# Optimization experiments

Hardware: AMD Instinct MI355X
Metric: run time of the kernel (lower is better)

## Reference

```python
import jax, jax.numpy as jnp
import numpy as np
import math

B, T, D = 4, 2048, 1024
NHEAD = 16
HEAD_DIM = D // NHEAD
MAX_REL = 16  # max_relative_position default


def setup_inputs() -> dict:
    key = jax.random.key(0)
    ks = jax.random.split(key, 10)
    s = 1.0 / math.sqrt(D)
    inp = {
        "x": jax.random.normal(ks[0], (B, T, D), dtype=jnp.float32),
        "Wq": jax.random.normal(ks[1], (D, D), dtype=jnp.float32) * s,
        "bq": jnp.zeros((D,), dtype=jnp.float32),
        "Wk": jax.random.normal(ks[2], (D, D), dtype=jnp.float32) * s,
        "bk": jnp.zeros((D,), dtype=jnp.float32),
        "Wv": jax.random.normal(ks[3], (D, D), dtype=jnp.float32) * s,
        "bv": jnp.zeros((D,), dtype=jnp.float32),
        "rel_bias": jax.random.normal(ks[4], (2 * MAX_REL - 1, NHEAD), dtype=jnp.float32) * 0.02,
        "Wo": jax.random.normal(ks[5], (D, D), dtype=jnp.float32) * s,
        "bo": jnp.zeros((D,), dtype=jnp.float32),
    }
    return inp


def _relative_bias(rel_bias, seq_len):
    # distance matrix clamped to [-(MAX_REL-1), MAX_REL-1], shifted to index table
    r = jnp.arange(seq_len)
    dist = jnp.clip(r[None, :] - r[:, None], -MAX_REL + 1, MAX_REL - 1) + MAX_REL - 1
    # gather: [T, T, H] -> [H, T, T]
    return jnp.transpose(rel_bias[dist], (2, 0, 1))


def reference(x, Wq, bq, Wk, bk, Wv, bv, rel_bias, Wo, bo):
    Bdim, Tdim, Ddim = x.shape
    # torch Linear: x @ W.T + b
    Q = x @ Wq.T + bq
    K = x @ Wk.T + bk
    V = x @ Wv.T + bv
    # [B, H, T, hd]
    Q = Q.reshape(Bdim, Tdim, NHEAD, HEAD_DIM).transpose(0, 2, 1, 3)
    K = K.reshape(Bdim, Tdim, NHEAD, HEAD_DIM).transpose(0, 2, 1, 3)
    V = V.reshape(Bdim, Tdim, NHEAD, HEAD_DIM).transpose(0, 2, 1, 3)
    scores = jnp.einsum("bhqd,bhkd->bhqk", Q, K) / math.sqrt(HEAD_DIM)
    scores = scores + _relative_bias(rel_bias, Tdim)[None]  # [1,H,T,T]
    attn = jax.nn.softmax(scores, axis=-1)
    out = jnp.einsum("bhqk,bhkd->bhqd", attn, V)
    out = out.transpose(0, 2, 1, 3).reshape(Bdim, Tdim, Ddim)
    return out @ Wo.T + bo
```

## Files before the change

kernel.cpp:

```cpp
#include <hip/hip_runtime.h>
#include <stdint.h>
#include <math.h>

typedef unsigned short u16;
typedef __bf16 bf16x8 __attribute__((ext_vector_type(8)));
typedef float f32x4 __attribute__((ext_vector_type(4)));
typedef float f32x2 __attribute__((ext_vector_type(2)));
typedef unsigned short u16x8 __attribute__((ext_vector_type(8)));
typedef unsigned short u16x4 __attribute__((ext_vector_type(4)));

#define BATCH 4
#define SEQT 2048
#define DMODEL 1024
#define NHEAD 16
#define HDIM 64
#define LOG2E 1.44269504f

#define LDS_GLD16(gp, lp)                                                     \
  __builtin_amdgcn_global_load_lds(                                           \
      (const __attribute__((address_space(1))) void*)(gp),                    \
      (__attribute__((address_space(3))) void*)(lp), 16, 0, 0)

static __device__ __forceinline__ u16 f2bf(float f) {
  union { float f; uint32_t u; } c; c.f = f;
  uint32_t u = c.u;
  return (u16)((u + 0x7fffu + ((u >> 16) & 1u)) >> 16);
}
static __device__ __forceinline__ u16 f2bf_fast(float f) {
  union { float f; uint32_t u; } c; c.f = f;
  return (u16)((c.u + 0x8000u) >> 16);
}
static __device__ __forceinline__ uint32_t pkbf(float a, float b) {
  union { float f; uint32_t u; } ca, cb; ca.f = a; cb.f = b;
  return __builtin_amdgcn_perm(cb.u + 0x8000u, ca.u + 0x8000u, 0x07060302u);
}

__global__ __launch_bounds__(256) void k_convert(const float* __restrict__ s,
                                                 u16* __restrict__ d, int n4) {
  int i = blockIdx.x * 256 + threadIdx.x;
  if (i >= n4) return;
  float4 v = ((const float4*)s)[i];
  u16x4 o = {f2bf(v.x), f2bf(v.y), f2bf(v.z), f2bf(v.w)};
  ((u16x4*)d)[i] = o;
}

__global__ __launch_bounds__(256) void k_gemm_qkv(
    const u16* __restrict__ A, const u16* __restrict__ W0,
    const u16* __restrict__ W1, const u16* __restrict__ W2,
    const float* __restrict__ b0, const float* __restrict__ b1,
    const float* __restrict__ b2, u16* __restrict__ dq, u16* __restrict__ dk,
    u16* __restrict__ dv) {
  __shared__ u16 As[128 * 64];
  __shared__ u16 Bs[128 * 64];

  const int z = blockIdx.z;
  const u16* Bm = z == 0 ? W0 : (z == 1 ? W1 : W2);
  const float* bias = z == 0 ? b0 : (z == 1 ? b1 : b2);
  u16* dst = z == 0 ? dq : (z == 1 ? dk : dv);

  const int tid = threadIdx.x;
  const int wave = tid >> 6, lane = tid & 63;
  const int quad = lane >> 4, l16 = lane & 15;
  const int wm = wave & 1, wn = wave >> 1;
  const int m0 = blockIdx.x * 128, n0 = blockIdx.y * 128;
  const int lrow = lane >> 3, lcol = (lane & 7) * 8;

  f32x4 acc[4][4] = {};

  for (int kt = 0; kt < 1024; kt += 64) {
    __syncthreads();
    for (int c = 0; c < 4; ++c) {
      int rr = (wave * 4 + c) * 8 + lrow;
      LDS_GLD16(A + (size_t)(m0 + rr) * 1024 + kt + lcol,
                &As[(wave * 4 + c) * 512]);
      LDS_GLD16(Bm + (size_t)(n0 + rr) * 1024 + kt + lcol,
                &Bs[(wave * 4 + c) * 512]);
    }
    __syncthreads();
    for (int kh = 0; kh < 2; ++kh) {
      bf16x8 af[4], bfr[4];
      for (int mt = 0; mt < 4; ++mt)
        af[mt] = *(const bf16x8*)&As[(wm * 64 + mt * 16 + l16) * 64 + kh * 32 +
                                     quad * 8];
      for (int nt = 0; nt < 4; ++nt)
        bfr[nt] = *(const bf16x8*)&Bs[(wn * 64 + nt * 16 + l16) * 64 + kh * 32 +
                                      quad * 8];
      for (int mt = 0; mt < 4; ++mt)
        for (int nt = 0; nt < 4; ++nt)
          acc[mt][nt] = __builtin_amdgcn_mfma_f32_16x16x32_bf16(
              af[mt], bfr[nt], acc[mt][nt], 0, 0, 0);
    }
  }

  for (int mt = 0; mt < 4; ++mt)
    for (int nt = 0; nt < 4; ++nt) {
      int n = n0 + wn * 64 + nt * 16 + l16;
      float bv = bias[n];
      int h = n >> 6, hd = n & 63;
      for (int r = 0; r < 4; ++r) {
        int m = m0 + wm * 64 + mt * 16 + quad * 4 + r;
        int b = m >> 11, t = m & 2047;
        float v = acc[mt][nt][r] + bv;
        dst[(((size_t)b * NHEAD + h) * SEQT + t) * HDIM + hd] = f2bf_fast(v);
      }
    }
}

__global__ __launch_bounds__(256) void k_gemm_proj(const u16* __restrict__ A,
                                                   const u16* __restrict__ Bm,
                                                   const float* __restrict__ bias,
                                                   float* __restrict__ out) {
  __shared__ u16 As[128 * 64];
  __shared__ u16 Bs[128 * 64];

  const int tid = threadIdx.x;
  const int wave = tid >> 6, lane = tid & 63;
  const int quad = lane >> 4, l16 = lane & 15;
  const int wm = wave & 1, wn = wave >> 1;
  const int m0 = blockIdx.x * 128, n0 = blockIdx.y * 128;
  const int lrow = lane >> 3, lcol = (lane & 7) * 8;

  f32x4 acc[4][4] = {};

  for (int kt = 0; kt < 1024; kt += 64) {
    __syncthreads();
    for (int c = 0; c < 4; ++c) {
      int rr = (wave * 4 + c) * 8 + lrow;
      LDS_GLD16(A + (size_t)(m0 + rr) * 1024 + kt + lcol,
                &As[(wave * 4 + c) * 512]);
      LDS_GLD16(Bm + (size_t)(n0 + rr) * 1024 + kt + lcol,
                &Bs[(wave * 4 + c) * 512]);
    }
    __syncthreads();
    for (int kh = 0; kh < 2; ++kh) {
      bf16x8 af[4], bfr[4];
      for (int mt = 0; mt < 4; ++mt)
        af[mt] = *(const bf16x8*)&As[(wm * 64 + mt * 16 + l16) * 64 + kh * 32 +
                                     quad * 8];
      for (int nt = 0; nt < 4; ++nt)
        bfr[nt] = *(const bf16x8*)&Bs[(wn * 64 + nt * 16 + l16) * 64 + kh * 32 +
                                      quad * 8];
      for (int mt = 0; mt < 4; ++mt)
        for (int nt = 0; nt < 4; ++nt)
          acc[mt][nt] = __builtin_amdgcn_mfma_f32_16x16x32_bf16(
              af[mt], bfr[nt], acc[mt][nt], 0, 0, 0);
    }
  }

  for (int mt = 0; mt < 4; ++mt)
    for (int nt = 0; nt < 4; ++nt) {
      int n = n0 + wn * 64 + nt * 16 + l16;
      float bv = bias[n];
      for (int r = 0; r < 4; ++r) {
        int m = m0 + wm * 64 + mt * 16 + quad * 4 + r;
        out[(size_t)m * 1024 + n] = acc[mt][nt][r] + bv;
      }
    }
}

__global__ __launch_bounds__(256) void k_attn(const u16* __restrict__ Qb,
                                              const u16* __restrict__ Kb,
                                              const u16* __restrict__ Vb,
                                              const float* __restrict__ relb,
                                              u16* __restrict__ Obf) {
  __shared__ u16 Ks[64 * 64];
  __shared__ u16 VTs[64 * 72];
  __shared__ u16 Ps[4][32 * 72];
  __shared__ float biasL[32];

  const int tid = threadIdx.x;
  const int wave = tid >> 6, lane = tid & 63;
  const int quad = lane >> 4, l16 = lane & 15;
  const int qt = blockIdx.x;
  const int bh = blockIdx.y;
  const int h = bh & (NHEAD - 1);
  const size_t base = (size_t)bh * SEQT * HDIM;
  const int q0 = qt * 128;
  const int qbase = q0 + wave * 32;

  if (tid < 31) biasL[tid] = relb[tid * NHEAD + h] * LOG2E;
  const float bLo = relb[0 * NHEAD + h] * LOG2E;
  const float bHi = relb[30 * NHEAD + h] * LOG2E;
  const float CL = 0.125f * LOG2E;

  bf16x8 bq[2][2];
  for (int qg = 0; qg < 2; ++qg) {
    const u16* qp = Qb + base + (size_t)(qbase + qg * 16 + l16) * HDIM;
    bq[qg][0] = *(const bf16x8*)(qp + quad * 8);
    bq[qg][1] = *(const bf16x8*)(qp + 32 + quad * 8);
  }

  f32x4 Oacc[4][2] = {};
  f32x2 ls2[2] = {};

  const int kp = tid >> 3;
  const int dgw = tid & 7;
  uint32_t* VT32 = (uint32_t*)VTs;

  for (int kt2 = 0; kt2 < 32; ++kt2) {
    const int k0 = kt2 * 64;
    __syncthreads();

    for (int c = 0; c < 2; ++c) {
      int rl = lane >> 3;
      int row = (wave * 2 + c) * 8 + rl;
      int gb = (lane & 7) ^ rl;
      LDS_GLD16(Kb + base + (size_t)(k0 + row) * HDIM + gb * 8,
                &Ks[(wave * 2 + c) * 512]);
    }
    {
      const u16* vp = Vb + base + (size_t)(k0 + 2 * kp) * HDIM + dgw * 8;
      u16x8 v0 = *(const u16x8*)vp;
      u16x8 v1 = *(const u16x8*)(vp + HDIM);
      const uint32_t* a32 = (const uint32_t*)&v0;
      const uint32_t* b32 = (const uint32_t*)&v1;
      int col = (((kp >> 2) ^ dgw) << 2) + (kp & 3);
      for (int j2 = 0; j2 < 4; ++j2) {
        uint32_t lo = __builtin_amdgcn_perm(a32[j2], b32[j2], 0x01000504u);
        uint32_t hi = __builtin_amdgcn_perm(a32[j2], b32[j2], 0x03020706u);
        int d0 = dgw * 8 + 2 * j2;
        VT32[d0 * 36 + col] = lo;
        VT32[(d0 + 1) * 36 + col] = hi;
      }
    }
    __syncthreads();

    for (int kg = 0; kg < 4; ++kg) {
      const int krow = kg * 16 + l16;
      const int sl = krow & 7;
      bf16x8 ak0 = *(const bf16x8*)&Ks[krow * 64 + ((quad ^ sl) << 3)];
      bf16x8 ak1 = *(const bf16x8*)&Ks[krow * 64 + (((quad + 4) ^ sl) << 3)];
      const int kb = k0 + kg * 16;
      for (int qg = 0; qg < 2; ++qg) {
        f32x4 s = {};
        s = __builtin_amdgcn_mfma_f32_16x16x32_bf16(ak0, bq[qg][0], s, 0, 0, 0);
        s = __builtin_amdgcn_mfma_f32_16x16x32_bf16(ak1, bq[qg][1], s, 0, 0, 0);
        const int qa = qbase + qg * 16;
        float p0, p1, p2, p3;
        const int dmin = kb - (qa + 15);
        const int dmax = kb + 15 - qa;
        if (dmin >= 15 || dmax <= -15) {
          const float ub = (dmin >= 15) ? bHi : bLo;
          p0 = __builtin_amdgcn_exp2f(fmaf(s[0], CL, ub));
          p1 = __builtin_amdgcn_exp2f(fmaf(s[1], CL, ub));
          p2 = __builtin_amdgcn_exp2f(fmaf(s[2], CL, ub));
          p3 = __builtin_amdgcn_exp2f(fmaf(s[3], CL, ub));
        } else {
          const int db = kb + quad * 4 - (qa + l16);
          float pv[4];
          for (int r = 0; r < 4; ++r) {
            int d = db + r;
            d = d < -15 ? -15 : (d > 15 ? 15 : d);
            pv[r] = __builtin_amdgcn_exp2f(fmaf(s[r], CL, biasL[d + 15]));
          }
          p0 = pv[0]; p1 = pv[1]; p2 = pv[2]; p3 = pv[3];
        }
        f32x2 t01 = {p0, p1}, t23 = {p2, p3};
        ls2[qg] += t01 + t23;
        uint2 w;
        w.x = pkbf(p0, p1);
        w.y = pkbf(p2, p3);
        *(uint2*)&Ps[wave][(qg * 16 + l16) * 72 + kg * 16 + quad * 4] = w;
      }
    }

    bf16x8 bp[2][2];
    for (int qg = 0; qg < 2; ++qg)
      for (int kh = 0; kh < 2; ++kh)
        bp[qg][kh] = *(const bf16x8*)&Ps[wave][(qg * 16 + l16) * 72 + kh * 32 +
                                              quad * 8];
    for (int dg = 0; dg < 4; ++dg) {
      const int d = dg * 16 + l16;
      const int g = d >> 3;
      bf16x8 av0 = *(const bf16x8*)&VTs[d * 72 + ((quad ^ g) << 3)];
      bf16x8 av1 = *(const bf16x8*)&VTs[d * 72 + (((quad + 4) ^ g) << 3)];
      for (int qg = 0; qg < 2; ++qg) {
        Oacc[dg][qg] = __builtin_amdgcn_mfma_f32_16x16x32_bf16(
            av0, bp[qg][0], Oacc[dg][qg], 0, 0, 0);
        Oacc[dg][qg] = __builtin_amdgcn_mfma_f32_16x16x32_bf16(
            av1, bp[qg][1], Oacc[dg][qg], 0, 0, 0);
      }
    }
  }

  float rinv[2];
  for (int qg = 0; qg < 2; ++qg) {
    float v = ls2[qg].x + ls2[qg].y;
    v += __shfl_xor(v, 16, 64);
    v += __shfl_xor(v, 32, 64);
    rinv[qg] = 1.0f / v;
  }

  const int b = bh >> 4;
  for (int dg = 0; dg < 4; ++dg)
    for (int qg = 0; qg < 2; ++qg) {
      int t = qbase + qg * 16 + l16;
      float o0 = Oacc[dg][qg][0] * rinv[qg];
      float o1 = Oacc[dg][qg][1] * rinv[qg];
      float o2 = Oacc[dg][qg][2] * rinv[qg];
      float o3 = Oacc[dg][qg][3] * rinv[qg];
      uint2 w;
      w.x = pkbf(o0, o1);
      w.y = pkbf(o2, o3);
      *(uint2*)(Obf + ((size_t)(b * SEQT + t)) * DMODEL + h * HDIM + dg * 16 +
                quad * 4) = w;
    }
}

extern "C" void kernel_launch(void* const* d_in, const int* in_sizes, int n_in,
                              void* d_out, int out_size, void* d_ws,
                              size_t ws_size, hipStream_t stream) {
  const float* x = (const float*)d_in[0];
  const float* Wq = (const float*)d_in[1];
  const float* bq = (const float*)d_in[2];
  const float* Wk = (const float*)d_in[3];
  const float* bk = (const float*)d_in[4];
  const float* Wv = (const float*)d_in[5];
  const float* bv = (const float*)d_in[6];
  const float* relb = (const float*)d_in[7];
  const float* Wo = (const float*)d_in[8];
  const float* bo = (const float*)d_in[9];
  float* out = (float*)d_out;

  char* ws = (char*)d_ws;
  const size_t SZ_X = (size_t)BATCH * SEQT * DMODEL * 2;
  const size_t SZ_W = (size_t)DMODEL * DMODEL * 2;
  u16* xbf = (u16*)(ws);
  u16* Wqb = (u16*)(ws + SZ_X);
  u16* Wkb = (u16*)(ws + SZ_X + SZ_W);
  u16* Wvb = (u16*)(ws + SZ_X + 2 * SZ_W);
  u16* Wob = (u16*)(ws + SZ_X + 3 * SZ_W);
  u16* Qb = (u16*)(ws + SZ_X + 4 * SZ_W);
  u16* Kb = (u16*)(ws + 2 * SZ_X + 4 * SZ_W);
  u16* Vb = (u16*)(ws + 3 * SZ_X + 4 * SZ_W);
  u16* Obf = (u16*)(ws + 4 * SZ_X + 4 * SZ_W);

  const int NX = BATCH * SEQT * DMODEL;
  const int NW = DMODEL * DMODEL;
  k_convert<<<NX / 4 / 256, 256, 0, stream>>>(x, xbf, NX / 4);
  k_convert<<<NW / 4 / 256, 256, 0, stream>>>(Wq, Wqb, NW / 4);
  k_convert<<<NW / 4 / 256, 256, 0, stream>>>(Wk, Wkb, NW / 4);
  k_convert<<<NW / 4 / 256, 256, 0, stream>>>(Wv, Wvb, NW / 4);
  k_convert<<<NW / 4 / 256, 256, 0, stream>>>(Wo, Wob, NW / 4);

  k_gemm_qkv<<<dim3(64, 8, 3), 256, 0, stream>>>(xbf, Wqb, Wkb, Wvb, bq, bk,
                                                 bv, Qb, Kb, Vb);
  k_attn<<<dim3(16, 64), 256, 0, stream>>>(Qb, Kb, Vb, relb, Obf);
  k_gemm_proj<<<dim3(64, 8), 256, 0, stream>>>(Obf, Wob, bo, out);
}
```

Measured before the change: 343.1 us.

## Produce transposed V from GEMM, widen attention to 512 threads, fuse converts

Merges the five fp32-to-bf16 conversion launches into one kernel. Splits the QKV projection into a Q/K GEMM and a separate V GEMM that writes V already transposed per head (Wv·xᵀ), so attention can load V tiles straight into LDS with async global-to-LDS loads instead of transposing with register permutes each iteration. Attention now runs 8 waves of 16 queries each instead of 4 waves of 32, which gives more waves per block at the cost of each K/V tile being reused across fewer queries per wave. The transposed V store in the GEMM epilogue writes scattered 2-byte values and may cost some write efficiency.

```diff
diff --git a/kernel.cpp b/kernel.cpp
--- a/kernel.cpp
+++ b/kernel.cpp
@@ -35,28 +35,36 @@
   return __builtin_amdgcn_perm(cb.u + 0x8000u, ca.u + 0x8000u, 0x07060302u);
 }
 
-__global__ __launch_bounds__(256) void k_convert(const float* __restrict__ s,
-                                                 u16* __restrict__ d, int n4) {
+__global__ __launch_bounds__(256) void k_convert_all(
+    const float* __restrict__ x, const float* __restrict__ Wq,
+    const float* __restrict__ Wk, const float* __restrict__ Wv,
+    const float* __restrict__ Wo, u16* __restrict__ xbf,
+    u16* __restrict__ Wqkv, u16* __restrict__ Wob) {
+  const int NX4 = 2097152, NW4 = 262144;
   int i = blockIdx.x * 256 + threadIdx.x;
-  if (i >= n4) return;
-  float4 v = ((const float4*)s)[i];
+  const float* s; u16* d; int js, jd;
+  if (i < NX4) {
+    s = x; d = xbf; js = jd = i;
+  } else if (i < NX4 + 3 * NW4) {
+    int j = i - NX4;
+    int w = j >> 18;
+    s = (w == 0) ? Wq : (w == 1) ? Wk : Wv;
+    js = j & (NW4 - 1);
+    d = Wqkv; jd = j;
+  } else {
+    s = Wo; d = Wob; js = jd = i - NX4 - 3 * NW4;
+  }
+  float4 v = ((const float4*)s)[js];
   u16x4 o = {f2bf(v.x), f2bf(v.y), f2bf(v.z), f2bf(v.w)};
-  ((u16x4*)d)[i] = o;
-}
-
-__global__ __launch_bounds__(256) void k_gemm_qkv(
-    const u16* __restrict__ A, const u16* __restrict__ W0,
-    const u16* __restrict__ W1, const u16* __restrict__ W2,
-    const float* __restrict__ b0, const float* __restrict__ b1,
-    const float* __restrict__ b2, u16* __restrict__ dq, u16* __restrict__ dk,
-    u16* __restrict__ dv) {
+  ((u16x4*)d)[jd] = o;
+}
+
+__global__ __launch_bounds__(256) void k_gemm_qk(
+    const u16* __restrict__ A, const u16* __restrict__ Bqk,
+    const float* __restrict__ bq_, const float* __restrict__ bk_,
+    u16* __restrict__ dq, u16* __restrict__ dk) {
   __shared__ u16 As[128 * 64];
   __shared__ u16 Bs[128 * 64];
-
-  const int z = blockIdx.z;
-  const u16* Bm = z == 0 ? W0 : (z == 1 ? W1 : W2);
-  const float* bias = z == 0 ? b0 : (z == 1 ? b1 : b2);
-  u16* dst = z == 0 ? dq : (z == 1 ? dk : dv);
 
   const int tid = threadIdx.x;
   const int wave = tid >> 6, lane = tid & 63;
@@ -73,7 +81,7 @@
       int rr = (wave * 4 + c) * 8 + lrow;
       LDS_GLD16(A + (size_t)(m0 + rr) * 1024 + kt + lcol,
                 &As[(wave * 4 + c) * 512]);
-      LDS_GLD16(Bm + (size_t)(n0 + rr) * 1024 + kt + lcol,
+      LDS_GLD16(Bqk + (size_t)(n0 + rr) * 1024 + kt + lcol,
                 &Bs[(wave * 4 + c) * 512]);
     }
     __syncthreads();
@@ -92,16 +100,75 @@
     }
   }
 
+  u16* dst = (n0 < 1024) ? dq : dk;
+  const float* bias = (n0 < 1024) ? bq_ : bk_;
+  for (int mt = 0; mt < 4; ++mt)
+    for (int nt = 0; nt < 4; ++nt) {
+      int nn = (n0 + wn * 64 + nt * 16 + l16) & 1023;
+      float bv = bias[nn];
+      int h = nn >> 6, hd = nn & 63;
+      for (int r = 0; r < 4; ++r) {
+        int m = m0 + wm * 64 + mt * 16 + quad * 4 + r;
+        int b = m >> 11, t = m & 2047;
+        dst[(((size_t)b * NHEAD + h) * SEQT + t) * HDIM + hd] =
+            f2bf_fast(acc[mt][nt][r] + bv);
+      }
+    }
+}
+
+__global__ __launch_bounds__(256) void k_gemm_vt(const u16* __restrict__ A,
+                                                 const u16* __restrict__ Bx,
+                                                 const float* __restrict__ bv_,
+                                                 u16* __restrict__ Vt) {
+  __shared__ u16 As[128 * 64];
+  __shared__ u16 Bs[128 * 64];
+  __shared__ float biasS[128];
+
+  const int tid = threadIdx.x;
+  const int wave = tid >> 6, lane = tid & 63;
+  const int quad = lane >> 4, l16 = lane & 15;
+  const int wm = wave & 1, wn = wave >> 1;
+  const int m0 = blockIdx.x * 128, n0 = blockIdx.y * 128;
+  const int lrow = lane >> 3, lcol = (lane & 7) * 8;
+
+  if (tid < 128) biasS[tid] = bv_[m0 + tid];
+
+  f32x4 acc[4][4] = {};
+
+  for (int kt = 0; kt < 1024; kt += 64) {
+    __syncthreads();
+    for (int c = 0; c < 4; ++c) {
+      int rr = (wave * 4 + c) * 8 + lrow;
+      LDS_GLD16(A + (size_t)(m0 + rr) * 1024 + kt + lcol,
+                &As[(wave * 4 + c) * 512]);
+      LDS_GLD16(Bx + (size_t)(n0 + rr) * 1024 + kt + lcol,
+                &Bs[(wave * 4 + c) * 512]);
+    }
+    __syncthreads();
+    for (int kh = 0; kh < 2; ++kh) {
+      bf16x8 af[4], bfr[4];
+      for (int mt = 0; mt < 4; ++mt)
+        af[mt] = *(const bf16x8*)&As[(wm * 64 + mt * 16 + l16) * 64 + kh * 32 +
+                                     quad * 8];
+      for (int nt = 0; nt < 4; ++nt)
+        bfr[nt] = *(const bf16x8*)&Bs[(wn * 64 + nt * 16 + l16) * 64 + kh * 32 +
+                                      quad * 8];
+      for (int mt = 0; mt < 4; ++mt)
+        for (int nt = 0; nt < 4; ++nt)
+          acc[mt][nt] = __builtin_amdgcn_mfma_f32_16x16x32_bf16(
+              af[mt], bfr[nt], acc[mt][nt], 0, 0, 0);
+    }
+  }
+
   for (int mt = 0; mt < 4; ++mt)
     for (int nt = 0; nt < 4; ++nt) {
       int n = n0 + wn * 64 + nt * 16 + l16;
-      float bv = bias[n];
-      int h = n >> 6, hd = n & 63;
+      int b = n >> 11, t = n & 2047;
       for (int r = 0; r < 4; ++r) {
         int m = m0 + wm * 64 + mt * 16 + quad * 4 + r;
-        int b = m >> 11, t = m & 2047;
-        float v = acc[mt][nt][r] + bv;
-        dst[(((size_t)b * NHEAD + h) * SEQT + t) * HDIM + hd] = f2bf_fast(v);
+        float v = acc[mt][nt][r] + biasS[m - m0];
+        Vt[((size_t)(b * NHEAD + (m >> 6)) * HDIM + (m & 63)) * SEQT + t] =
+            f2bf_fast(v);
       }
     }
 }
@@ -158,14 +225,14 @@
     }
 }
 
-__global__ __launch_bounds__(256) void k_attn(const u16* __restrict__ Qb,
-                                              const u16* __restrict__ Kb,
-                                              const u16* __restrict__ Vb,
-                                              const float* __restrict__ relb,
-                                              u16* __restrict__ Obf) {
+__global__ __launch_bounds__(512, 8) void k_attn(const u16* __restrict__ Qb,
+                                                 const u16* __restrict__ Kb,
+                                                 const u16* __restrict__ Vt,
+                                                 const float* __restrict__ relb,
+                                                 u16* __restrict__ Obf) {
   __shared__ u16 Ks[64 * 64];
-  __shared__ u16 VTs[64 * 72];
-  __shared__ u16 Ps[4][32 * 72];
+  __shared__ u16 VTs[64 * 64];
+  __shared__ u16 Ps[8][16 * 72];
   __shared__ float biasL[32];
 
   const int tid = threadIdx.x;
@@ -176,135 +243,99 @@
   const int h = bh & (NHEAD - 1);
   const size_t base = (size_t)bh * SEQT * HDIM;
   const int q0 = qt * 128;
-  const int qbase = q0 + wave * 32;
+  const int qa = q0 + wave * 16;
 
   if (tid < 31) biasL[tid] = relb[tid * NHEAD + h] * LOG2E;
   const float bLo = relb[0 * NHEAD + h] * LOG2E;
   const float bHi = relb[30 * NHEAD + h] * LOG2E;
   const float CL = 0.125f * LOG2E;
 
-  bf16x8 bq[2][2];
-  for (int qg = 0; qg < 2; ++qg) {
-    const u16* qp = Qb + base + (size_t)(qbase + qg * 16 + l16) * HDIM;
-    bq[qg][0] = *(const bf16x8*)(qp + quad * 8);
-    bq[qg][1] = *(const bf16x8*)(qp + 32 + quad * 8);
-  }
-
-  f32x4 Oacc[4][2] = {};
-  f32x2 ls2[2] = {};
-
-  const int kp = tid >> 3;
-  const int dgw = tid & 7;
-  uint32_t* VT32 = (uint32_t*)VTs;
+  bf16x8 bq0, bq1;
+  {
+    const u16* qp = Qb + base + (size_t)(qa + l16) * HDIM;
+    bq0 = *(const bf16x8*)(qp + quad * 8);
+    bq1 = *(const bf16x8*)(qp + 32 + quad * 8);
+  }
+
+  f32x4 Oacc[4] = {};
+  f32x2 ls2 = {};
+
+  const int rl = lane >> 3;
+  const int gb = (lane & 7) ^ rl;
+  const int srow = wave * 8 + rl;
+  const u16* kgp = Kb + base + (size_t)srow * HDIM + gb * 8;
+  const u16* vgp = Vt + base + (size_t)srow * SEQT + gb * 8;
+  u16* ksl = &Ks[wave * 512];
+  u16* vsl = &VTs[wave * 512];
+  const int sl = l16 & 7;
 
   for (int kt2 = 0; kt2 < 32; ++kt2) {
     const int k0 = kt2 * 64;
     __syncthreads();
-
-    for (int c = 0; c < 2; ++c) {
-      int rl = lane >> 3;
-      int row = (wave * 2 + c) * 8 + rl;
-      int gb = (lane & 7) ^ rl;
-      LDS_GLD16(Kb + base + (size_t)(k0 + row) * HDIM + gb * 8,
-                &Ks[(wave * 2 + c) * 512]);
-    }
-    {
-      const u16* vp = Vb + base + (size_t)(k0 + 2 * kp) * HDIM + dgw * 8;
-      u16x8 v0 = *(const u16x8*)vp;
-      u16x8 v1 = *(const u16x8*)(vp + HDIM);
-      const uint32_t* a32 = (const uint32_t*)&v0;
-      const uint32_t* b32 = (const uint32_t*)&v1;
-      int col = (((kp >> 2) ^ dgw) << 2) + (kp & 3);
-      for (int j2 = 0; j2 < 4; ++j2) {
-        uint32_t lo = __builtin_amdgcn_perm(a32[j2], b32[j2], 0x01000504u);
-        uint32_t hi = __builtin_amdgcn_perm(a32[j2], b32[j2], 0x03020706u);
-        int d0 = dgw * 8 + 2 * j2;
-        VT32[d0 * 36 + col] = lo;
-        VT32[(d0 + 1) * 36 + col] = hi;
-      }
-    }
+    LDS_GLD16(kgp + (size_t)k0 * HDIM, ksl);
+    LDS_GLD16(vgp + k0, vsl);
     __syncthreads();
 
     for (int kg = 0; kg < 4; ++kg) {
       const int krow = kg * 16 + l16;
-      const int sl = krow & 7;
       bf16x8 ak0 = *(const bf16x8*)&Ks[krow * 64 + ((quad ^ sl) << 3)];
-      bf16x8 ak1 = *(const bf16x8*)&Ks[krow * 64 + (((quad + 4) ^ sl) << 3)];
+      bf16x8 ak1 = *(const bf16x8*)&Ks[krow * 64 + (((4 + quad) ^ sl) << 3)];
+      f32x4 s = {};
+      s = __builtin_amdgcn_mfma_f32_16x16x32_bf16(ak0, bq0, s, 0, 0, 0);
+      s = __builtin_amdgcn_mfma_f32_16x16x32_bf16(ak1, bq1, s, 0, 0, 0);
       const int kb = k0 + kg * 16;
-      for (int qg = 0; qg < 2; ++qg) {
-        f32x4 s = {};
-        s = __builtin_amdgcn_mfma_f32_16x16x32_bf16(ak0, bq[qg][0], s, 0, 0, 0);
-        s = __builtin_amdgcn_mfma_f32_16x16x32_bf16(ak1, bq[qg][1], s, 0, 0, 0);
-        const int qa = qbase + qg * 16;
-        float p0, p1, p2, p3;
-        const int dmin = kb - (qa + 15);
-        const int dmax = kb + 15 - qa;
-        if (dmin >= 15 || dmax <= -15) {
-          const float ub = (dmin >= 15) ? bHi : bLo;
-          p0 = __builtin_amdgcn_exp2f(fmaf(s[0], CL, ub));
-          p1 = __builtin_amdgcn_exp2f(fmaf(s[1], CL, ub));
-          p2 = __builtin_amdgcn_exp2f(fmaf(s[2], CL, ub));
-          p3 = __builtin_amdgcn_exp2f(fmaf(s[3], CL, ub));
-        } else {
-          const int db = kb + quad * 4 - (qa + l16);
-          float pv[4];
-          for (int r = 0; r < 4; ++r) {
-            int d = db + r;
-            d = d < -15 ? -15 : (d > 15 ? 15 : d);
-            pv[r] = __builtin_amdgcn_exp2f(fmaf(s[r], CL, biasL[d + 15]));
-          }
-          p0 = pv[0]; p1 = pv[1]; p2 = pv[2]; p3 = pv[3];
+      float p0, p1, p2, p3;
+      const int dmin = kb - (qa + 15);
+      const int dmax = kb + 15 - qa;
+      if (dmin >= 15 || dmax <= -15) {
+        const float ub = (dmin >= 15) ? bHi : bLo;
+        p0 = __builtin_amdgcn_exp2f(fmaf(s[0], CL, ub));
+        p1 = __builtin_amdgcn_exp2f(fmaf(s[1], CL, ub));
+        p2 = __builtin_amdgcn_exp2f(fmaf(s[2], CL, ub));
+        p3 = __builtin_amdgcn_exp2f(fmaf(s[3], CL, ub));
+      } else {
+        const int db = kb + quad * 4 - (qa + l16);
+        float pv[4];
+        for (int r = 0; r < 4; ++r) {
+          int d = db + r;
+          d = d < -15 ? -15 : (d > 15 ? 15 : d);
+          pv[r] = __builtin_amdgcn_exp2f(fmaf(s[r], CL, biasL[d + 15]));
         }
-        f32x2 t01 = {p0, p1}, t23 = {p2, p3};
-        ls2[qg] += t01 + t23;
-        uint2 w;
-        w.x = pkbf(p0, p1);
-        w.y = pkbf(p2, p3);
-        *(uint2*)&Ps[wave][(qg * 16 + l16) * 72 + kg * 16 + quad * 4] = w;
+        p0 = pv[0]; p1 = pv[1]; p2 = pv[2]; p3 = pv[3];
       }
-    }
-
-    bf16x8 bp[2][2];
-    for (int qg = 0; qg < 2; ++qg)
-      for (int kh = 0; kh < 2; ++kh)
-        bp[qg][kh] = *(const bf16x8*)&Ps[wave][(qg * 16 + l16) * 72 + kh * 32 +
-                                              quad * 8];
+      f32x2 t01 = {p0, p1}, t23 = {p2, p3};
+      ls2 += t01 + t23;
+      uint2 w;
+      w.x = pkbf(p0, p1);
+      w.y = pkbf(p2, p3);
+      *(uint2*)&Ps[wave][l16 * 72 + kg * 16 + quad * 4] = w;
+    }
+
+    bf16x8 bp0 = *(const bf16x8*)&Ps[wave][l16 * 72 + quad * 8];
+    bf16x8 bp1 = *(const bf16x8*)&Ps[wave][l16 * 72 + 32 + quad * 8];
     for (int dg = 0; dg < 4; ++dg) {
       const int d = dg * 16 + l16;
-      const int g = d >> 3;
-      bf16x8 av0 = *(const bf16x8*)&VTs[d * 72 + ((quad ^ g) << 3)];
-      bf16x8 av1 = *(const bf16x8*)&VTs[d * 72 + (((quad + 4) ^ g) << 3)];
-      for (int qg = 0; qg < 2; ++qg) {
-        Oacc[dg][qg] = __builtin_amdgcn_mfma_f32_16x16x32_bf16(
-            av0, bp[qg][0], Oacc[dg][qg], 0, 0, 0);
-        Oacc[dg][qg] = __builtin_amdgcn_mfma_f32_16x16x32_bf16(
-            av1, bp[qg][1], Oacc[dg][qg], 0, 0, 0);
-      }
-    }
-  }
-
-  float rinv[2];
-  for (int qg = 0; qg < 2; ++qg) {
-    float v = ls2[qg].x + ls2[qg].y;
-    v += __shfl_xor(v, 16, 64);
-    v += __shfl_xor(v, 32, 64);
-    rinv[qg] = 1.0f / v;
-  }
+      bf16x8 av0 = *(const bf16x8*)&VTs[d * 64 + ((quad ^ sl) << 3)];
+      bf16x8 av1 = *(const bf16x8*)&VTs[d * 64 + (((4 + quad) ^ sl) << 3)];
+      Oacc[dg] = __builtin_amdgcn_mfma_f32_16x16x32_bf16(av0, bp0, Oacc[dg], 0, 0, 0);
+      Oacc[dg] = __builtin_amdgcn_mfma_f32_16x16x32_bf16(av1, bp1, Oacc[dg], 0, 0, 0);
+    }
+  }
+
+  float v = ls2.x + ls2.y;
+  v += __shfl_xor(v, 16, 64);
+  v += __shfl_xor(v, 32, 64);
+  const float rinv = 1.0f / v;
 
   const int b = bh >> 4;
-  for (int dg = 0; dg < 4; ++dg)
-    for (int qg = 0; qg < 2; ++qg) {
-      int t = qbase + qg * 16 + l16;
-      float o0 = Oacc[dg][qg][0] * rinv[qg];
-      float o1 = Oacc[dg][qg][1] * rinv[qg];
-      float o2 = Oacc[dg][qg][2] * rinv[qg];
-      float o3 = Oacc[dg][qg][3] * rinv[qg];
-      uint2 w;
-      w.x = pkbf(o0, o1);
-      w.y = pkbf(o2, o3);
-      *(uint2*)(Obf + ((size_t)(b * SEQT + t)) * DMODEL + h * HDIM + dg * 16 +
-                quad * 4) = w;
-    }
+  const int t = qa + l16;
+  u16* op = Obf + ((size_t)(b * SEQT + t)) * DMODEL + h * HDIM;
+  for (int dg = 0; dg < 4; ++dg) {
+    uint2 w;
+    w.x = pkbf(Oacc[dg][0] * rinv, Oacc[dg][1] * rinv);
+    w.y = pkbf(Oacc[dg][2] * rinv, Oacc[dg][3] * rinv);
+    *(uint2*)(op + dg * 16 + quad * 4) = w;
+  }
 }
 
 extern "C" void kernel_launch(void* const* d_in, const int* in_sizes, int n_in,
@@ -327,24 +358,16 @@
   const size_t SZ_W = (size_t)DMODEL * DMODEL * 2;
   u16* xbf = (u16*)(ws);
   u16* Wqb = (u16*)(ws + SZ_X);
-  u16* Wkb = (u16*)(ws + SZ_X + SZ_W);
   u16* Wvb = (u16*)(ws + SZ_X + 2 * SZ_W);
   u16* Wob = (u16*)(ws + SZ_X + 3 * SZ_W);
   u16* Qb = (u16*)(ws + SZ_X + 4 * SZ_W);
   u16* Kb = (u16*)(ws + 2 * SZ_X + 4 * SZ_W);
-  u16* Vb = (u16*)(ws + 3 * SZ_X + 4 * SZ_W);
+  u16* Vt = (u16*)(ws + 3 * SZ_X + 4 * SZ_W);
   u16* Obf = (u16*)(ws + 4 * SZ_X + 4 * SZ_W);
 
-  const int NX = BATCH * SEQT * DMODEL;
-  const int NW = DMODEL * DMODEL;
-  k_convert<<<NX / 4 / 256, 256, 0, stream>>>(x, xbf, NX / 4);
-  k_convert<<<NW / 4 / 256, 256, 0, stream>>>(Wq, Wqb, NW / 4);
-  k_convert<<<NW / 4 / 256, 256, 0, stream>>>(Wk, Wkb, NW / 4);
-  k_convert<<<NW / 4 / 256, 256, 0, stream>>>(Wv, Wvb, NW / 4);
-  k_convert<<<NW / 4 / 256, 256, 0, stream>>>(Wo, Wob, NW / 4);
-
-  k_gemm_qkv<<<dim3(64, 8, 3), 256, 0, stream>>>(xbf, Wqb, Wkb, Wvb, bq, bk,
-                                                 bv, Qb, Kb, Vb);
-  k_attn<<<dim3(16, 64), 256, 0, stream>>>(Qb, Kb, Vb, relb, Obf);
+  k_convert_all<<<12288, 256, 0, stream>>>(x, Wq, Wk, Wv, Wo, xbf, Wqb, Wob);
+  k_gemm_qk<<<dim3(64, 16), 256, 0, stream>>>(xbf, Wqb, bq, bk, Qb, Kb);
+  k_gemm_vt<<<dim3(8, 64), 256, 0, stream>>>(Wvb, xbf, bv, Vt);
+  k_attn<<<dim3(16, 64), 512, 0, stream>>>(Qb, Kb, Vt, relb, Obf);
   k_gemm_proj<<<dim3(64, 8), 256, 0, stream>>>(Obf, Wob, bo, out);
 }
```

After: 323.1 us. 5.8% less time.
